# Optimization experiments

Measured on AMD Instinct MI355X. Metric: run time of the kernel, lower is better.

Reference implementation:

```python
import jax, jax.numpy as jnp
import numpy as np

V = 32000   # vocab_size
B = 32      # batch_size
T = 128     # seq_length
R = 1024    # rnn_size
L = 4       # effective layers: layer_depth**2 due to double MultiRNNCell wrap in source
EPS = 1e-5
FORGET_BIAS = 1.0


def setup_inputs() -> dict:
    key = jax.random.key(0)
    ks = jax.random.split(key, 5)
    return {
        "input_data": jax.random.randint(ks[0], (B, T), 0, V),
        "embedding": jax.random.uniform(ks[1], (V, R), minval=-1.0, maxval=1.0, dtype=jnp.float32),
        "W": jax.random.normal(ks[2], (L, 2 * R, 4 * R), dtype=jnp.float32) * 0.02,
        "bias": jnp.zeros((L, 4 * R), jnp.float32),
        "ln_g": jnp.ones((L, 5, R), jnp.float32),   # LN scale for i, j, f, o, new_c
        "ln_b": jnp.zeros((L, 5, R), jnp.float32),  # LN shift for i, j, f, o, new_c
        "softmax_w": jax.random.normal(ks[3], (V, R), dtype=jnp.float32) * 0.02,
        "softmax_b": jnp.zeros((V,), jnp.float32),
    }


def _ln(x, g, b):
    m = jnp.mean(x, axis=-1, keepdims=True)
    v = jnp.var(x, axis=-1, keepdims=True)
    return (x - m) * jax.lax.rsqrt(v + EPS) * g + b


def _ln_lstm_layer(xs, W, bias, g, bt):
    """LayerNormalizedLSTMCell scanned over time. xs: [T, B, R] -> [T, B, R]."""
    def step(carry, x):
        c, h = carry
        z = jnp.concatenate([x, h], axis=-1) @ W + bias  # [B, 4R]
        i, j, f, o = jnp.split(z, 4, axis=-1)
        i = _ln(i, g[0], bt[0])
        j = _ln(j, g[1], bt[1])
        f = _ln(f, g[2], bt[2])
        o = _ln(o, g[3], bt[3])
        c = c * jax.nn.sigmoid(f + FORGET_BIAS) + jax.nn.sigmoid(i) * jnp.tanh(j)
        h = jnp.tanh(_ln(c, g[4], bt[4])) * jax.nn.sigmoid(o)
        return (c, h), h

    z0 = jnp.zeros(xs.shape[1:], xs.dtype)
    _, ys = jax.lax.scan(step, (z0, z0), xs)
    return ys


def reference(input_data, embedding, W, bias, ln_g, ln_b, softmax_w, softmax_b):
    xs = embedding[input_data]                 # [B, T, R]
    xs = jnp.transpose(xs, (1, 0, 2))          # [T, B, R] time-major for scan
    for l in range(L):
        xs = _ln_lstm_layer(xs, W[l], bias[l], ln_g[l], ln_b[l])
    out = jnp.transpose(xs, (1, 0, 2)).reshape(-1, R)       # [B*T, R]
    logits = out @ softmax_w.T + softmax_b                  # [B*T, V]
    return logits
```

## Files before the change

### kernel.cpp

```cpp
#include <hip/hip_runtime.h>
#include <hip/hip_bf16.h>


typedef __bf16 bf16x8 __attribute__((ext_vector_type(8)));
typedef __bf16 bf16x4 __attribute__((ext_vector_type(4)));
typedef float  f32x4  __attribute__((ext_vector_type(4)));

#define VOCAB 32000
#define BATCH 32
#define SEQ   128
#define RNN   1024
#define NLAY  4
#define GBLK  128
#define AR_STRIDE 16
#define NTILES_N 250
#define NTILES_T 32
#define NTILES  (NTILES_N * NTILES_T)

__device__ __forceinline__ float sigm(float x) { return 1.f / (1.f + __expf(-x)); }

__device__ __forceinline__ unsigned ald(const unsigned* p) {
    return __hip_atomic_load(p, __ATOMIC_RELAXED, __HIP_MEMORY_SCOPE_AGENT);
}
__device__ __forceinline__ void ast(unsigned* p, unsigned v) {
    __hip_atomic_store(p, v, __ATOMIC_RELAXED, __HIP_MEMORY_SCOPE_AGENT);
}
__device__ __forceinline__ unsigned long long ald64(const unsigned long long* p) {
    return __hip_atomic_load(p, __ATOMIC_RELAXED, __HIP_MEMORY_SCOPE_AGENT);
}
__device__ __forceinline__ void ast64(unsigned long long* p, unsigned long long v) {
    __hip_atomic_store(p, v, __ATOMIC_RELAXED, __HIP_MEMORY_SCOPE_AGENT);
}
__device__ __forceinline__ void astf(float* p, float v) {
    __hip_atomic_store(p, v, __ATOMIC_RELAXED, __HIP_MEMORY_SCOPE_AGENT);
}
__device__ __forceinline__ void drain_vm() {
    asm volatile("s_waitcnt vmcnt(0)" ::: "memory");
}

typedef union { unsigned long long u[2]; f32x4 f; }  U128F;
typedef union { unsigned long long u; bf16x4 v; }    U64B;

__global__ __launch_bounds__(256) void k_cvt_w(const float* __restrict__ W,
                                               __bf16* __restrict__ Wt) {
    __shared__ float lds[64][65];
    const int tid = threadIdx.x, tx = tid & 15, ty = tid >> 4;
    const int n0 = blockIdx.x * 64, k0 = blockIdx.y * 64;
    const size_t l = blockIdx.z;
    const float* src = W + (l * 2048 + (size_t)k0) * 4096 + n0;
#pragma unroll
    for (int rr = 0; rr < 4; ++rr) {
        int kr = rr * 16 + ty;
        f32x4 v = *(const f32x4*)(src + (size_t)kr * 4096 + tx * 4);
        lds[kr][tx*4+0] = v[0]; lds[kr][tx*4+1] = v[1];
        lds[kr][tx*4+2] = v[2]; lds[kr][tx*4+3] = v[3];
    }
    __syncthreads();
    __bf16* dhi = Wt + ((l * 2 + 0) * 4096 + (size_t)n0) * 2048 + k0;
    __bf16* dlo = Wt + ((l * 2 + 1) * 4096 + (size_t)n0) * 2048 + k0;
#pragma unroll
    for (int rr = 0; rr < 4; ++rr) {
        int nr = rr * 16 + ty;
        bf16x4 ohi, olo;
#pragma unroll
        for (int j = 0; j < 4; ++j) {
            float x = lds[tx*4+j][nr];
            __bf16 h = (__bf16)x;
            ohi[j] = h;
            olo[j] = (__bf16)(x - (float)h);
        }
        *(bf16x4*)(dhi + (size_t)nr * 2048 + tx * 4) = ohi;
        *(bf16x4*)(dlo + (size_t)nr * 2048 + tx * 4) = olo;
    }
}

__global__ __launch_bounds__(256) void k_cvt(const float* __restrict__ in,
                                             __bf16* __restrict__ out) {
    size_t i = ((size_t)blockIdx.x * 256 + threadIdx.x) * 8;
    f32x4 v0 = *(const f32x4*)(in + i);
    f32x4 v1 = *(const f32x4*)(in + i + 4);
    bf16x8 o;
    o[0]=(__bf16)v0[0]; o[1]=(__bf16)v0[1]; o[2]=(__bf16)v0[2]; o[3]=(__bf16)v0[3];
    o[4]=(__bf16)v1[0]; o[5]=(__bf16)v1[1]; o[6]=(__bf16)v1[2]; o[7]=(__bf16)v1[3];
    *(bf16x8*)(out + i) = o;
}

__global__ __launch_bounds__(256) void k_embed(const int* __restrict__ idx,
                                               const float* __restrict__ emb,
                                               __bf16* __restrict__ xhi,
                                               __bf16* __restrict__ xlo) {
    const int row = blockIdx.x;
    const int t = row >> 5, b = row & 31;
    const int id = idx[b * SEQ + t];
    const int tid = threadIdx.x;
    f32x4 v = *(const f32x4*)(emb + (size_t)id * RNN + tid * 4);
    bf16x4 hi, lo;
#pragma unroll
    for (int j = 0; j < 4; ++j) {
        __bf16 h = (__bf16)v[j];
        hi[j] = h; lo[j] = (__bf16)(v[j] - (float)h);
    }
    *(bf16x4*)(xhi + (size_t)row * RNN + tid * 4) = hi;
    *(bf16x4*)(xlo + (size_t)row * RNN + tid * 4) = lo;
}

__global__ __launch_bounds__(256) void k_xgemm(const __bf16* __restrict__ xhi,
                                               const __bf16* __restrict__ xlo,
                                               const __bf16* __restrict__ Wt,
                                               const float* __restrict__ bias,
                                               float* __restrict__ zx) {
    __shared__ __bf16 Aim[2][4][4][512];
    __shared__ __bf16 Bim[2][4][4][512];
    const int tid = threadIdx.x;
    const int lane = tid & 63, w = tid >> 6;
    const int g = lane >> 4, q = lane & 15;
    const int n0 = blockIdx.x * 64, m0 = blockIdx.y * 64;
    f32x4 acc[4] = {{0,0,0,0},{0,0,0,0},{0,0,0,0},{0,0,0,0}};

    for (int ch = 0; ch < 8; ++ch) {
        __syncthreads();
        for (int i = tid; i < 2048; i += 256) {
            int pl = i >> 10, rem = i & 1023;
            int r = rem >> 4, cc = rem & 15;
            const __bf16* s = (pl ? xlo : xhi) + (size_t)(m0 + r) * RNN + ch * 128 + cc * 8;
            bf16x8 v = *(const bf16x8*)s;
            *(bf16x8*)&Aim[pl][r >> 4][cc >> 2][(((cc & 3) << 4) + (r & 15)) << 3] = v;
        }
        for (int i = tid; i < 2048; i += 256) {
            int pl = i >> 10, rem = i & 1023;
            int r = rem >> 4, cc = rem & 15;
            const __bf16* s = Wt + ((size_t)(pl ? 4096 : 0) + n0 + r) * 2048 + ch * 128 + cc * 8;
            bf16x8 v = *(const bf16x8*)s;
            *(bf16x8*)&Bim[pl][r >> 4][cc >> 2][(((cc & 3) << 4) + (r & 15)) << 3] = v;
        }
        __syncthreads();
#pragma unroll
        for (int kc = 0; kc < 4; ++kc) {
            bf16x8 bhf = *(const bf16x8*)&Bim[0][w][kc][lane << 3];
            bf16x8 blf = *(const bf16x8*)&Bim[1][w][kc][lane << 3];
#pragma unroll
            for (int mt = 0; mt < 4; ++mt) {
                bf16x8 ahf = *(const bf16x8*)&Aim[0][mt][kc][lane << 3];
                bf16x8 alf = *(const bf16x8*)&Aim[1][mt][kc][lane << 3];
                acc[mt] = __builtin_amdgcn_mfma_f32_16x16x32_bf16(ahf, bhf, acc[mt], 0, 0, 0);
                acc[mt] = __builtin_amdgcn_mfma_f32_16x16x32_bf16(alf, bhf, acc[mt], 0, 0, 0);
                acc[mt] = __builtin_amdgcn_mfma_f32_16x16x32_bf16(ahf, blf, acc[mt], 0, 0, 0);
            }
        }
    }
    const int n = n0 + w * 16 + q;
    const float bv = bias[n];
#pragma unroll
    for (int mt = 0; mt < 4; ++mt)
#pragma unroll
        for (int r = 0; r < 4; ++r) {
            int m = m0 + mt * 16 + g * 4 + r;
            zx[(size_t)m * 4096 + n] = acc[mt][r] + bv;
        }
}

__device__ __forceinline__ void bar_all(unsigned* slots, int bk, int tid,
                                        unsigned gen, bool poll) {
    drain_vm();
    __syncthreads();
    if (tid == 0) ast(&slots[bk * AR_STRIDE], gen);
    if (poll && tid < GBLK) {
        while (ald(&slots[tid * AR_STRIDE]) < gen) __builtin_amdgcn_s_sleep(1);
    }
    __syncthreads();
}
__device__ __forceinline__ void bar_gate(unsigned* slots, int bk, bool arrive,
                                         int tid, unsigned gen) {
    drain_vm();
    __syncthreads();
    if (arrive && tid == 0) ast(&slots[bk * AR_STRIDE], gen);
    if (tid < BATCH) {
        while (ald(&slots[tid * AR_STRIDE]) < gen) __builtin_amdgcn_s_sleep(1);
    }
    __syncthreads();
}

__global__ __launch_bounds__(256, 1) void k_rnn(
        const __bf16* __restrict__ Wl,
        float* __restrict__ zx,
        float* __restrict__ z,
        __bf16* __restrict__ xhi, __bf16* __restrict__ xlo,
        const float* __restrict__ g5, const float* __restrict__ b5,
        unsigned* bar, unsigned gen0,
        const __bf16* __restrict__ Wn,
        const float* __restrict__ bias_n,
        int mode,
        const __bf16* __restrict__ pw,
        const float* __restrict__ psb,
        float* __restrict__ pout)
{
    __shared__ __bf16 wl[2][32768];
    __shared__ f32x4 pred[2][2][64];
    __shared__ float red[4][8];
    unsigned* bar2 = bar + GBLK * AR_STRIDE;

    const int bk = blockIdx.x, tid = threadIdx.x;
    const int lane = tid & 63, w = tid >> 6;
    const int q = lane & 15, g = lane >> 4;
    const int mt = w & 1, kh = w >> 1;
    const int zr0  = (mt << 4) + (g << 2);

    if (bk >= GBLK) {
        if (mode == 1) {
            __bf16* As = &wl[0][0];
            __bf16* Bs = &wl[0][16384];
            const int wm = w & 1, wn = w >> 1;
            const int lr = lane >> 2, cc4 = lane & 3;
            const int gidx = cc4 * 16 + lr;
            for (int tau = bk - GBLK; tau < NTILES; tau += GBLK) {
                const int tt = tau / NTILES_N;
                const int n0p = (tau - tt * NTILES_N) * 128;
                const unsigned gneed = gen0 + 4u * (unsigned)tt + 4u;
                if (tid < BATCH) {
                    while (ald(&bar2[tid * AR_STRIDE]) < gneed)
                        __builtin_amdgcn_s_sleep(1);
                }
                __syncthreads();
                const __bf16* asrc[2];
                const __bf16* bsrc[2];
#pragma unroll
                for (int p2 = 0; p2 < 2; ++p2) {
                    int st = p2 * 4 + w;
                    asrc[p2] = xhi + (size_t)(tt * 128 + st * 16 + lr) * RNN + cc4 * 8;
                    bsrc[p2] = pw  + (size_t)(n0p + st * 16 + lr) * RNN + cc4 * 8;
                }
                f32x4 acc[4][4];
#pragma unroll
                for (int i = 0; i < 4; ++i)
#pragma unroll
                    for (int j = 0; j < 4; ++j) acc[i][j] = (f32x4){0.f,0.f,0.f,0.f};
                bf16x8 ar[2], br[2];
#pragma unroll
                for (int p2 = 0; p2 < 2; ++p2) {
                    ar[p2] = *(const bf16x8*)(asrc[p2]);
                    br[p2] = *(const bf16x8*)(bsrc[p2]);
                }
#pragma unroll
                for (int p2 = 0; p2 < 2; ++p2) {
                    int st = p2 * 4 + w;
                    *(bf16x8*)&As[st * 512 + gidx * 8] = ar[p2];
                    *(bf16x8*)&Bs[st * 512 + gidx * 8] = br[p2];
                }
                __syncthreads();
                for (int s = 0; s < 32; ++s) {
                    const int buf = s & 1;
                    if (s + 1 < 32) {
                        const int k0 = (s + 1) * 32;
#pragma unroll
                        for (int p2 = 0; p2 < 2; ++p2) {
                            ar[p2] = *(const bf16x8*)(asrc[p2] + k0);
                            br[p2] = *(const bf16x8*)(bsrc[p2] + k0);
                        }
                    }
                    bf16x8 af[4], bfr[4];
#pragma unroll
                    for (int i = 0; i < 4; ++i) {
                        af[i]  = *(const bf16x8*)&As[(buf * 8 + wm * 4 + i) * 512 + lane * 8];
                        bfr[i] = *(const bf16x8*)&Bs[(buf * 8 + wn * 4 + i) * 512 + lane * 8];
                    }
#pragma unroll
                    for (int mi = 0; mi < 4; ++mi)
#pragma unroll
                        for (int ni = 0; ni < 4; ++ni)
                            acc[mi][ni] = __builtin_amdgcn_mfma_f32_16x16x32_bf16(
                                af[mi], bfr[ni], acc[mi][ni], 0, 0, 0);
                    if (s + 1 < 32) {
#pragma unroll
                        for (int p2 = 0; p2 < 2; ++p2) {
                            int st = p2 * 4 + w;
                            *(bf16x8*)&As[((buf ^ 1) * 8 + st) * 512 + gidx * 8] = ar[p2];
                            *(bf16x8*)&Bs[((buf ^ 1) * 8 + st) * 512 + gidx * 8] = br[p2];
                        }
                    }
                    __syncthreads();
                }
#pragma unroll
                for (int ni = 0; ni < 4; ++ni) {
                    const int n = n0p + wn * 64 + ni * 16 + q;
                    const float bv = psb[n];
#pragma unroll
                    for (int mi = 0; mi < 4; ++mi) {
                        const int rb = wm * 64 + mi * 16 + g * 4;
#pragma unroll
                        for (int r = 0; r < 4; ++r) {
                            const int R = tt * 128 + rb + r;
                            const int m = (R & 31) * 128 + (R >> 5);
                            __builtin_nontemporal_store(acc[mi][ni][r] + bv,
                                                        &pout[(size_t)m * VOCAB + n]);
                        }
                    }
                }
            }
            return;
        }
        const int hk = bk - GBLK;
        const int ncolh = (hk << 5) + q;
        {
            const __bf16* hi_src = Wn + ((size_t)(hk << 5)) * 2048;
            const __bf16* lo_src = Wn + ((size_t)(4096 + (hk << 5))) * 2048;
            for (int i = tid; i < 8192; i += 256) {
                int pl = i >> 12, rem = i & 4095;
                int r = rem >> 7, cc = rem & 127;
                const __bf16* s = (pl ? lo_src : hi_src) + (size_t)r * 2048 + cc * 8;
                bf16x8 v = *(const bf16x8*)s;
                int rnt = r >> 4, rq = r & 15, kc = cc >> 2, rg = cc & 3;
                *(bf16x8*)&wl[pl][((rnt * 32 + kc) << 9) + ((rg * 16 + rq) << 3)] = v;
            }
        }
        float bv0 = 0.f, bv1 = 0.f;
        if (kh == 0) { bv0 = bias_n[ncolh]; bv1 = bias_n[ncolh + 16]; }
        __syncthreads();
        const __bf16* hb0 = &wl[0][0]        + (lane << 3);
        const __bf16* lb0 = &wl[1][0]        + (lane << 3);
        const __bf16* hb1 = &wl[0][32 << 9]  + (lane << 3);
        const __bf16* lb1 = &wl[1][32 << 9]  + (lane << 3);

        for (int t = 0; t < SEQ; ++t) {
            const unsigned gen = gen0 + (unsigned)t + 1u;
            if (tid < BATCH) {
                while (ald(&bar2[tid * AR_STRIDE]) < gen) __builtin_amdgcn_s_sleep(1);
            }
            __syncthreads();
            const __bf16* ah = xhi + ((size_t)t * BATCH + (mt << 4) + q) * RNN;
            const __bf16* al = xlo + ((size_t)t * BATCH + (mt << 4) + q) * RNN;
            f32x4 a00={0,0,0,0}, a01={0,0,0,0}, a02={0,0,0,0};
            f32x4 a10={0,0,0,0}, a11={0,0,0,0}, a12={0,0,0,0};
            const int k0 = kh << 4;
#pragma unroll 4
            for (int kc = k0; kc < k0 + 16; ++kc) {
                bf16x8 ahf = *(const bf16x8*)(ah + (kc << 5) + (g << 3));
                bf16x8 alf = *(const bf16x8*)(al + (kc << 5) + (g << 3));
                bf16x8 b0h = *(const bf16x8*)(hb0 + (kc << 9));
                bf16x8 b0l = *(const bf16x8*)(lb0 + (kc << 9));
                bf16x8 b1h = *(const bf16x8*)(hb1 + (kc << 9));
                bf16x8 b1l = *(const bf16x8*)(lb1 + (kc << 9));
                a00 = __builtin_amdgcn_mfma_f32_16x16x32_bf16(ahf, b0h, a00, 0, 0, 0);
                a01 = __builtin_amdgcn_mfma_f32_16x16x32_bf16(alf, b0h, a01, 0, 0, 0);
                a02 = __builtin_amdgcn_mfma_f32_16x16x32_bf16(ahf, b0l, a02, 0, 0, 0);
                a10 = __builtin_amdgcn_mfma_f32_16x16x32_bf16(ahf, b1h, a10, 0, 0, 0);
                a11 = __builtin_amdgcn_mfma_f32_16x16x32_bf16(alf, b1h, a11, 0, 0, 0);
                a12 = __builtin_amdgcn_mfma_f32_16x16x32_bf16(ahf, b1l, a12, 0, 0, 0);
            }
            f32x4 s0, s1;
#pragma unroll
            for (int j = 0; j < 4; ++j) {
                s0[j] = a00[j] + a01[j] + a02[j];
                s1[j] = a10[j] + a11[j] + a12[j];
            }
            if (kh == 1) { pred[mt][0][lane] = s0; pred[mt][1][lane] = s1; }
            __syncthreads();
            if (kh == 0) {
                f32x4 p0 = pred[mt][0][lane], p1 = pred[mt][1][lane];
#pragma unroll
                for (int r = 0; r < 4; ++r) {
                    zx[((size_t)t * BATCH + zr0 + r) * 4096 + ncolh]      = s0[r] + p0[r] + bv0;
                    zx[((size_t)t * BATCH + zr0 + r) * 4096 + ncolh + 16] = s1[r] + p1[r] + bv1;
                }
            }
            __syncthreads();
        }
        return;
    }

    const int ncol = (bk << 5) + q;

    {
        const __bf16* hi_src = Wl + ((size_t)(bk << 5)) * 2048 + RNN;
        const __bf16* lo_src = Wl + ((size_t)(4096 + (bk << 5))) * 2048 + RNN;
        for (int i = tid; i < 8192; i += 256) {
            int pl = i >> 12, rem = i & 4095;
            int r = rem >> 7, cc = rem & 127;
            const __bf16* s = (pl ? lo_src : hi_src) + (size_t)r * 2048 + cc * 8;
            bf16x8 v = *(const bf16x8*)s;
            int rnt = r >> 4, rq = r & 15, kc = cc >> 2, rg = cc & 3;
            *(bf16x8*)&wl[pl][((rnt * 32 + kc) << 9) + ((rg * 16 + rq) << 3)] = v;
        }
    }

    const bool is_gate = (bk < BATCH);
    f32x4 gi, bi, gj, bj, gf, bfv, go, bo, g4, b4;
    if (is_gate) {
        gi = *(const f32x4*)(g5 + 0*RNN + tid*4); bi = *(const f32x4*)(b5 + 0*RNN + tid*4);
        gj = *(const f32x4*)(g5 + 1*RNN + tid*4); bj = *(const f32x4*)(b5 + 1*RNN + tid*4);
        gf = *(const f32x4*)(g5 + 2*RNN + tid*4); bfv= *(const f32x4*)(b5 + 2*RNN + tid*4);
        go = *(const f32x4*)(g5 + 3*RNN + tid*4); bo = *(const f32x4*)(b5 + 3*RNN + tid*4);
        g4 = *(const f32x4*)(g5 + 4*RNN + tid*4); b4 = *(const f32x4*)(b5 + 4*RNN + tid*4);
    }
    const float inv = 1.f / (float)RNN;
    f32x4 creg = {0.f, 0.f, 0.f, 0.f};
    __syncthreads();

    const __bf16* bh0 = &wl[0][0]        + (lane << 3);
    const __bf16* bl0 = &wl[1][0]        + (lane << 3);
    const __bf16* bh1 = &wl[0][32 << 9]  + (lane << 3);
    const __bf16* bl1 = &wl[1][32 << 9]  + (lane << 3);

    float zv0[4], zv1[4];
    if (kh == 0) {
        const float* zxp = zx + (size_t)zr0 * 4096 + ncol;
#pragma unroll
        for (int r = 0; r < 4; ++r) {
            zv0[r] = zxp[(size_t)r * 4096];
            zv1[r] = zxp[(size_t)r * 4096 + 16];
        }
    }

    for (int t = 0; t < SEQ; ++t) {
        const unsigned gen = gen0 + (unsigned)t + 1u;
        f32x4 a00={0,0,0,0}, a01={0,0,0,0}, a02={0,0,0,0};
        f32x4 a10={0,0,0,0}, a11={0,0,0,0}, a12={0,0,0,0};
        if (t > 0) {
            const __bf16* ah = xhi + ((size_t)(t - 1) * BATCH + (mt << 4) + q) * RNN;
            const __bf16* al = xlo + ((size_t)(t - 1) * BATCH + (mt << 4) + q) * RNN;
            const int k0 = kh << 4;
#pragma unroll 4
            for (int kc = k0; kc < k0 + 16; ++kc) {
                bf16x8 ahf = *(const bf16x8*)(ah + (kc << 5) + (g << 3));
                bf16x8 alf = *(const bf16x8*)(al + (kc << 5) + (g << 3));
                bf16x8 b0h = *(const bf16x8*)(bh0 + (kc << 9));
                bf16x8 b0l = *(const bf16x8*)(bl0 + (kc << 9));
                bf16x8 b1h = *(const bf16x8*)(bh1 + (kc << 9));
                bf16x8 b1l = *(const bf16x8*)(bl1 + (kc << 9));
                a00 = __builtin_amdgcn_mfma_f32_16x16x32_bf16(ahf, b0h, a00, 0, 0, 0);
                a01 = __builtin_amdgcn_mfma_f32_16x16x32_bf16(alf, b0h, a01, 0, 0, 0);
                a02 = __builtin_amdgcn_mfma_f32_16x16x32_bf16(ahf, b0l, a02, 0, 0, 0);
                a10 = __builtin_amdgcn_mfma_f32_16x16x32_bf16(ahf, b1h, a10, 0, 0, 0);
                a11 = __builtin_amdgcn_mfma_f32_16x16x32_bf16(alf, b1h, a11, 0, 0, 0);
                a12 = __builtin_amdgcn_mfma_f32_16x16x32_bf16(ahf, b1l, a12, 0, 0, 0);
            }
        }
        {
            f32x4 s0, s1;
#pragma unroll
            for (int j = 0; j < 4; ++j) {
                s0[j] = a00[j] + a01[j] + a02[j];
                s1[j] = a10[j] + a11[j] + a12[j];
            }
            if (kh == 1) { pred[mt][0][lane] = s0; pred[mt][1][lane] = s1; }
            __syncthreads();
            if (kh == 0) {
                f32x4 p0 = pred[mt][0][lane], p1 = pred[mt][1][lane];
#pragma unroll
                for (int r = 0; r < 4; ++r) {
                    astf(&z[(size_t)(zr0 + r) * 4096 + ncol],      s0[r] + p0[r] + zv0[r]);
                    astf(&z[(size_t)(zr0 + r) * 4096 + ncol + 16], s1[r] + p1[r] + zv1[r]);
                }
            }
        }
        bar_all(bar, bk, tid, gen, is_gate);

        if (kh == 0 && t + 1 < SEQ) {
            const float* zxp = zx + ((size_t)(t + 1) * BATCH + zr0) * 4096 + ncol;
#pragma unroll
            for (int r = 0; r < 4; ++r) {
                zv0[r] = zxp[(size_t)r * 4096];
                zv1[r] = zxp[(size_t)r * 4096 + 16];
            }
        }

        if (is_gate) {
            const int b = bk;
            const float* zrow = z + (size_t)b * 4096 + tid * 4;
            auto ld4 = [&](const float* p) -> f32x4 {
                U128F x;
                x.u[0] = ald64((const unsigned long long*)p);
                x.u[1] = ald64((const unsigned long long*)p + 1);
                return x.f;
            };
            f32x4 zi = ld4(zrow), zjv = ld4(zrow + 1024),
                  zfv = ld4(zrow + 2048), zov = ld4(zrow + 3072);
            float s[8];
            s[0] = zi[0]+zi[1]+zi[2]+zi[3];
            s[1] = zi[0]*zi[0]+zi[1]*zi[1]+zi[2]*zi[2]+zi[3]*zi[3];
            s[2] = zjv[0]+zjv[1]+zjv[2]+zjv[3];
            s[3] = zjv[0]*zjv[0]+zjv[1]*zjv[1]+zjv[2]*zjv[2]+zjv[3]*zjv[3];
            s[4] = zfv[0]+zfv[1]+zfv[2]+zfv[3];
            s[5] = zfv[0]*zfv[0]+zfv[1]*zfv[1]+zfv[2]*zfv[2]+zfv[3]*zfv[3];
            s[6] = zov[0]+zov[1]+zov[2]+zov[3];
            s[7] = zov[0]*zov[0]+zov[1]*zov[1]+zov[2]*zov[2]+zov[3]*zov[3];
#pragma unroll
            for (int o = 32; o; o >>= 1)
#pragma unroll
                for (int i = 0; i < 8; ++i) s[i] += __shfl_xor(s[i], o);
            if (lane == 0) {
#pragma unroll
                for (int i = 0; i < 8; ++i) red[w][i] = s[i];
            }
            __syncthreads();
            float tot[8];
#pragma unroll
            for (int i = 0; i < 8; ++i) tot[i] = red[0][i]+red[1][i]+red[2][i]+red[3][i];

            float mi = tot[0]*inv, ri = rsqrtf(tot[1]*inv - mi*mi + 1e-5f);
            float mj = tot[2]*inv, rj = rsqrtf(tot[3]*inv - mj*mj + 1e-5f);
            float mf = tot[4]*inv, rf = rsqrtf(tot[5]*inv - mf*mf + 1e-5f);
            float mo = tot[6]*inv, ro = rsqrtf(tot[7]*inv - mo*mo + 1e-5f);

            f32x4 onrm;
            float cs = 0.f, cq = 0.f;
#pragma unroll
            for (int j = 0; j < 4; ++j) {
                float iv = (zi[j]-mi)*ri*gi[j] + bi[j];
                float jv = (zjv[j]-mj)*rj*gj[j] + bj[j];
                float fv = (zfv[j]-mf)*rf*gf[j] + bfv[j];
                float ov = (zov[j]-mo)*ro*go[j] + bo[j];
                float cc = creg[j] * sigm(fv + 1.0f) + sigm(iv) * tanhf(jv);
                creg[j] = cc; onrm[j] = ov;
                cs += cc; cq += cc*cc;
            }

            __syncthreads();
            float s2a = cs, s2b = cq;
#pragma unroll
            for (int o = 32; o; o >>= 1) { s2a += __shfl_xor(s2a, o); s2b += __shfl_xor(s2b, o); }
            if (lane == 0) { red[w][0] = s2a; red[w][1] = s2b; }
            __syncthreads();
            float mc = (red[0][0]+red[1][0]+red[2][0]+red[3][0]) * inv;
            float vc = (red[0][1]+red[1][1]+red[2][1]+red[3][1]) * inv - mc*mc;
            float rc = rsqrtf(vc + 1e-5f);

            bf16x4 hh, hl;
#pragma unroll
            for (int j = 0; j < 4; ++j) {
                float cn = (creg[j]-mc)*rc*g4[j] + b4[j];
                float h = tanhf(cn) * sigm(onrm[j]);
                __bf16 a = (__bf16)h;
                hh[j] = a; hl[j] = (__bf16)(h - (float)a);
            }
            U64B ph, pl;
            ph.v = hh; pl.v = hl;
            ast64((unsigned long long*)&xhi[((size_t)t * BATCH + b) * RNN + tid * 4], ph.u);
            ast64((unsigned long long*)&xlo[((size_t)t * BATCH + b) * RNN + tid * 4], pl.u);
        }
        bar_gate(bar2, bk, is_gate, tid, gen);
    }
}

extern "C" void kernel_launch(void* const* d_in, const int* in_sizes, int n_in,
                              void* d_out, int out_size, void* d_ws, size_t ws_size,
                              hipStream_t stream) {
    const int*   input = (const int*)  d_in[0];
    const float* emb   = (const float*)d_in[1];
    const float* W     = (const float*)d_in[2];
    const float* bias  = (const float*)d_in[3];
    const float* ln_g  = (const float*)d_in[4];
    const float* ln_b  = (const float*)d_in[5];
    const float* smw   = (const float*)d_in[6];
    const float* smb   = (const float*)d_in[7];
    float* out = (float*)d_out;

    char* p = (char*)d_ws;
    auto alloc = [&](size_t bytes) { char* r = p; p += (bytes + 255) & ~(size_t)255; return r; };
    __bf16* Wt   = (__bf16*)alloc((size_t)NLAY * 2 * 4096 * 2048 * 2);
    __bf16* smwb = (__bf16*)alloc((size_t)VOCAB * RNN * 2);
    __bf16* xhi  = (__bf16*)alloc((size_t)SEQ * BATCH * RNN * 2);
    __bf16* xlo  = (__bf16*)alloc((size_t)SEQ * BATCH * RNN * 2);
    float*  zx   = (float*) alloc((size_t)SEQ * BATCH * 4096 * 4);
    float*  z    = (float*) alloc((size_t)BATCH * 4096 * 4);
    unsigned* bar= (unsigned*)alloc(2 * GBLK * AR_STRIDE * 4);

    hipMemsetAsync(bar, 0, 2 * GBLK * AR_STRIDE * 4, stream);

    k_cvt_w<<<dim3(64, 32, NLAY), 256, 0, stream>>>(W, Wt);
    k_cvt<<<(VOCAB * RNN) / (8 * 256), 256, 0, stream>>>(smw, smwb);
    k_embed<<<SEQ * BATCH, 256, 0, stream>>>(input, emb, xhi, xlo);

    k_xgemm<<<dim3(64, 64), 256, 0, stream>>>(xhi, xlo, Wt, bias, zx);

    for (int l = 0; l < NLAY; ++l) {
        const __bf16* Wl  = Wt + (size_t)l * 2 * 4096 * 2048;
        const float*  gl  = ln_g + (size_t)l * 5 * RNN;
        const float*  bbl = ln_b + (size_t)l * 5 * RNN;
        const int lnext = (l + 1 < NLAY) ? (l + 1) : l;
        const __bf16* Wn  = Wt + (size_t)lnext * 2 * 4096 * 2048;
        const float*  bn  = bias + (size_t)lnext * 4096;
        {
            const __bf16* Wl_ = Wl;
            float* zx_ = zx;
            float* z_ = z;
            __bf16 *xhi_ = xhi, *xlo_ = xlo;
            const float *gl_ = gl, *bbl_ = bbl;
            unsigned* bar_ = bar;
            unsigned gen0 = (unsigned)(l * SEQ);
            const __bf16* Wn_ = Wn;
            const float* bn_ = bn;
            int mode = (l + 1 < NLAY) ? 0 : 1;
            const __bf16* pw_ = smwb;
            const float* psb_ = smb;
            float* pout_ = out;
            void* args[] = {(void*)&Wl_, (void*)&zx_, (void*)&z_,
                            (void*)&xhi_, (void*)&xlo_, (void*)&gl_, (void*)&bbl_,
                            (void*)&bar_, (void*)&gen0, (void*)&Wn_, (void*)&bn_,
                            (void*)&mode, (void*)&pw_, (void*)&psb_, (void*)&pout_};
            hipLaunchCooperativeKernel((const void*)k_rnn,
                                       dim3(2 * GBLK), dim3(256), args, 0, stream);
        }
    }
}
```

Before: 5.746 ms.

## Fuse layer-0 input projection into recurrent kernel helper blocks with per-step flags

```diff
diff --git a/kernel.cpp b/kernel.cpp
--- a/kernel.cpp
+++ b/kernel.cpp
@@ -104,61 +104,6 @@
     *(bf16x4*)(xlo + (size_t)row * RNN + tid * 4) = lo;
 }
 
-__global__ __launch_bounds__(256) void k_xgemm(const __bf16* __restrict__ xhi,
-                                               const __bf16* __restrict__ xlo,
-                                               const __bf16* __restrict__ Wt,
-                                               const float* __restrict__ bias,
-                                               float* __restrict__ zx) {
-    __shared__ __bf16 Aim[2][4][4][512];
-    __shared__ __bf16 Bim[2][4][4][512];
-    const int tid = threadIdx.x;
-    const int lane = tid & 63, w = tid >> 6;
-    const int g = lane >> 4, q = lane & 15;
-    const int n0 = blockIdx.x * 64, m0 = blockIdx.y * 64;
-    f32x4 acc[4] = {{0,0,0,0},{0,0,0,0},{0,0,0,0},{0,0,0,0}};
-
-    for (int ch = 0; ch < 8; ++ch) {
-        __syncthreads();
-        for (int i = tid; i < 2048; i += 256) {
-            int pl = i >> 10, rem = i & 1023;
-            int r = rem >> 4, cc = rem & 15;
-            const __bf16* s = (pl ? xlo : xhi) + (size_t)(m0 + r) * RNN + ch * 128 + cc * 8;
-            bf16x8 v = *(const bf16x8*)s;
-            *(bf16x8*)&Aim[pl][r >> 4][cc >> 2][(((cc & 3) << 4) + (r & 15)) << 3] = v;
-        }
-        for (int i = tid; i < 2048; i += 256) {
-            int pl = i >> 10, rem = i & 1023;
-            int r = rem >> 4, cc = rem & 15;
-            const __bf16* s = Wt + ((size_t)(pl ? 4096 : 0) + n0 + r) * 2048 + ch * 128 + cc * 8;
-            bf16x8 v = *(const bf16x8*)s;
-            *(bf16x8*)&Bim[pl][r >> 4][cc >> 2][(((cc & 3) << 4) + (r & 15)) << 3] = v;
-        }
-        __syncthreads();
-#pragma unroll
-        for (int kc = 0; kc < 4; ++kc) {
-            bf16x8 bhf = *(const bf16x8*)&Bim[0][w][kc][lane << 3];
-            bf16x8 blf = *(const bf16x8*)&Bim[1][w][kc][lane << 3];
-#pragma unroll
-            for (int mt = 0; mt < 4; ++mt) {
-                bf16x8 ahf = *(const bf16x8*)&Aim[0][mt][kc][lane << 3];
-                bf16x8 alf = *(const bf16x8*)&Aim[1][mt][kc][lane << 3];
-                acc[mt] = __builtin_amdgcn_mfma_f32_16x16x32_bf16(ahf, bhf, acc[mt], 0, 0, 0);
-                acc[mt] = __builtin_amdgcn_mfma_f32_16x16x32_bf16(alf, bhf, acc[mt], 0, 0, 0);
-                acc[mt] = __builtin_amdgcn_mfma_f32_16x16x32_bf16(ahf, blf, acc[mt], 0, 0, 0);
-            }
-        }
-    }
-    const int n = n0 + w * 16 + q;
-    const float bv = bias[n];
-#pragma unroll
-    for (int mt = 0; mt < 4; ++mt)
-#pragma unroll
-        for (int r = 0; r < 4; ++r) {
-            int m = m0 + mt * 16 + g * 4 + r;
-            zx[(size_t)m * 4096 + n] = acc[mt][r] + bv;
-        }
-}
-
 __device__ __forceinline__ void bar_all(unsigned* slots, int bk, int tid,
                                         unsigned gen, bool poll) {
     drain_vm();
@@ -189,6 +134,7 @@
         unsigned* bar, unsigned gen0,
         const __bf16* __restrict__ Wn,
         const float* __restrict__ bias_n,
+        const float* __restrict__ bias_l,
         int mode,
         const __bf16* __restrict__ pw,
         const float* __restrict__ psb,
@@ -198,6 +144,7 @@
     __shared__ f32x4 pred[2][2][64];
     __shared__ float red[4][8];
     unsigned* bar2 = bar + GBLK * AR_STRIDE;
+    unsigned* bar3 = bar + 2 * GBLK * AR_STRIDE;
 
     const int bk = blockIdx.x, tid = threadIdx.x;
     const int lane = tid & 63, w = tid >> 6;
@@ -300,6 +247,71 @@
         }
         const int hk = bk - GBLK;
         const int ncolh = (hk << 5) + q;
+
+        if (mode == 2) {
+            {
+                const __bf16* hi_src = Wl + ((size_t)(hk << 5)) * 2048;
+                const __bf16* lo_src = Wl + ((size_t)(4096 + (hk << 5))) * 2048;
+                for (int i = tid; i < 8192; i += 256) {
+                    int pl = i >> 12, rem = i & 4095;
+                    int r = rem >> 7, cc = rem & 127;
+                    const __bf16* s = (pl ? lo_src : hi_src) + (size_t)r * 2048 + cc * 8;
+                    bf16x8 v = *(const bf16x8*)s;
+                    int rnt = r >> 4, rq = r & 15, kc = cc >> 2, rg = cc & 3;
+                    *(bf16x8*)&wl[pl][((rnt * 32 + kc) << 9) + ((rg * 16 + rq) << 3)] = v;
+                }
+            }
+            float bv0 = 0.f, bv1 = 0.f;
+            if (kh == 0) { bv0 = bias_l[ncolh]; bv1 = bias_l[ncolh + 16]; }
+            __syncthreads();
+            const __bf16* hb0 = &wl[0][0]        + (lane << 3);
+            const __bf16* lb0 = &wl[1][0]        + (lane << 3);
+            const __bf16* hb1 = &wl[0][32 << 9]  + (lane << 3);
+            const __bf16* lb1 = &wl[1][32 << 9]  + (lane << 3);
+            for (int t = 0; t < SEQ; ++t) {
+                const __bf16* ah = xhi + ((size_t)t * BATCH + (mt << 4) + q) * RNN;
+                const __bf16* al = xlo + ((size_t)t * BATCH + (mt << 4) + q) * RNN;
+                f32x4 a00={0,0,0,0}, a01={0,0,0,0}, a02={0,0,0,0};
+                f32x4 a10={0,0,0,0}, a11={0,0,0,0}, a12={0,0,0,0};
+                const int k0 = kh << 4;
+#pragma unroll 4
+                for (int kc = k0; kc < k0 + 16; ++kc) {
+                    bf16x8 ahf = *(const bf16x8*)(ah + (kc << 5) + (g << 3));
+                    bf16x8 alf = *(const bf16x8*)(al + (kc << 5) + (g << 3));
+                    bf16x8 b0h = *(const bf16x8*)(hb0 + (kc << 9));
+                    bf16x8 b0l = *(const bf16x8*)(lb0 + (kc << 9));
+                    bf16x8 b1h = *(const bf16x8*)(hb1 + (kc << 9));
+                    bf16x8 b1l = *(const bf16x8*)(lb1 + (kc << 9));
+                    a00 = __builtin_amdgcn_mfma_f32_16x16x32_bf16(ahf, b0h, a00, 0, 0, 0);
+                    a01 = __builtin_amdgcn_mfma_f32_16x16x32_bf16(alf, b0h, a01, 0, 0, 0);
+                    a02 = __builtin_amdgcn_mfma_f32_16x16x32_bf16(ahf, b0l, a02, 0, 0, 0);
+                    a10 = __builtin_amdgcn_mfma_f32_16x16x32_bf16(ahf, b1h, a10, 0, 0, 0);
+                    a11 = __builtin_amdgcn_mfma_f32_16x16x32_bf16(alf, b1h, a11, 0, 0, 0);
+                    a12 = __builtin_amdgcn_mfma_f32_16x16x32_bf16(ahf, b1l, a12, 0, 0, 0);
+                }
+                f32x4 s0, s1;
+#pragma unroll
+                for (int j = 0; j < 4; ++j) {
+                    s0[j] = a00[j] + a01[j] + a02[j];
+                    s1[j] = a10[j] + a11[j] + a12[j];
+                }
+                if (kh == 1) { pred[mt][0][lane] = s0; pred[mt][1][lane] = s1; }
+                __syncthreads();
+                if (kh == 0) {
+                    f32x4 p0 = pred[mt][0][lane], p1 = pred[mt][1][lane];
+#pragma unroll
+                    for (int r = 0; r < 4; ++r) {
+                        astf(&zx[((size_t)t * BATCH + zr0 + r) * 4096 + ncolh],      s0[r] + p0[r] + bv0);
+                        astf(&zx[((size_t)t * BATCH + zr0 + r) * 4096 + ncolh + 16], s1[r] + p1[r] + bv1);
+                    }
+                }
+                drain_vm();
+                __syncthreads();
+                if (tid == 0) ast(&bar3[hk * AR_STRIDE], (unsigned)(t + 1));
+            }
+            __syncthreads();
+        }
+
         {
             const __bf16* hi_src = Wn + ((size_t)(hk << 5)) * 2048;
             const __bf16* lo_src = Wn + ((size_t)(4096 + (hk << 5))) * 2048;
@@ -402,6 +414,9 @@
 
     float zv0[4], zv1[4];
     if (kh == 0) {
+        if (mode == 2) {
+            while (ald(&bar3[bk * AR_STRIDE]) < 1u) __builtin_amdgcn_s_sleep(1);
+        }
         const float* zxp = zx + (size_t)zr0 * 4096 + ncol;
 #pragma unroll
         for (int r = 0; r < 4; ++r) {
@@ -455,6 +470,10 @@
         bar_all(bar, bk, tid, gen, is_gate);
 
         if (kh == 0 && t + 1 < SEQ) {
+            if (mode == 2) {
+                while (ald(&bar3[bk * AR_STRIDE]) < (unsigned)(t + 2))
+                    __builtin_amdgcn_s_sleep(1);
+            }
             const float* zxp = zx + ((size_t)(t + 1) * BATCH + zr0) * 4096 + ncol;
 #pragma unroll
             for (int r = 0; r < 4; ++r) {
@@ -562,15 +581,13 @@
     __bf16* xlo  = (__bf16*)alloc((size_t)SEQ * BATCH * RNN * 2);
     float*  zx   = (float*) alloc((size_t)SEQ * BATCH * 4096 * 4);
     float*  z    = (float*) alloc((size_t)BATCH * 4096 * 4);
-    unsigned* bar= (unsigned*)alloc(2 * GBLK * AR_STRIDE * 4);
-
-    hipMemsetAsync(bar, 0, 2 * GBLK * AR_STRIDE * 4, stream);
+    unsigned* bar= (unsigned*)alloc(3 * GBLK * AR_STRIDE * 4);
+
+    hipMemsetAsync(bar, 0, 3 * GBLK * AR_STRIDE * 4, stream);
 
     k_cvt_w<<<dim3(64, 32, NLAY), 256, 0, stream>>>(W, Wt);
     k_cvt<<<(VOCAB * RNN) / (8 * 256), 256, 0, stream>>>(smw, smwb);
     k_embed<<<SEQ * BATCH, 256, 0, stream>>>(input, emb, xhi, xlo);
-
-    k_xgemm<<<dim3(64, 64), 256, 0, stream>>>(xhi, xlo, Wt, bias, zx);
 
     for (int l = 0; l < NLAY; ++l) {
         const __bf16* Wl  = Wt + (size_t)l * 2 * 4096 * 2048;
@@ -589,13 +606,15 @@
             unsigned gen0 = (unsigned)(l * SEQ);
             const __bf16* Wn_ = Wn;
             const float* bn_ = bn;
-            int mode = (l + 1 < NLAY) ? 0 : 1;
+            const float* bl_ = bias + (size_t)l * 4096;
+            int mode = (l == 0) ? 2 : ((l + 1 < NLAY) ? 0 : 1);
             const __bf16* pw_ = smwb;
             const float* psb_ = smb;
             float* pout_ = out;
             void* args[] = {(void*)&Wl_, (void*)&zx_, (void*)&z_,
                             (void*)&xhi_, (void*)&xlo_, (void*)&gl_, (void*)&bbl_,
                             (void*)&bar_, (void*)&gen0, (void*)&Wn_, (void*)&bn_,
+                            (void*)&bl_,
                             (void*)&mode, (void*)&pw_, (void*)&psb_, (void*)&pout_};
             hipLaunchCooperativeKernel((const void*)k_rnn,
                                        dim3(2 * GBLK), dim3(256), args, 0, stream);
```

After: 5.372 ms. 6.5% less time.
